# Kernel tuning notes

Measured on AMD Instinct MI355X. Metric: run time of the kernel, lower is better.

The kernel has to match this reference:

```python
import jax, jax.numpy as jnp
import numpy as np
import math

E = 1024   # embedding_size
H = 16     # layer_size (num heads)
DK = 64    # key_size
DH = 64    # head_size
HID = 4096 # hidden_size
B = 2
S = 2048   # context_size
EPS = 1e-5


def layer_norm(x, w, b):
    mu = jnp.mean(x, axis=-1, keepdims=True)
    var = jnp.mean(jnp.square(x - mu), axis=-1, keepdims=True)
    return (x - mu) * jax.lax.rsqrt(var + EPS) * w + b


def setup_inputs() -> dict:
    key = jax.random.key(0)
    ks = jax.random.split(key, 16)
    sE = 1.0 / math.sqrt(E)
    sH = 1.0 / math.sqrt(HID)
    return {
        "embeddings": jax.random.normal(ks[0], (B, S, E), dtype=jnp.float32),
        "Wq": jax.random.uniform(ks[1], (H, E, DK), minval=-sE, maxval=sE, dtype=jnp.float32),
        "bq": jnp.zeros((H, DK), dtype=jnp.float32),
        "Wk": jax.random.uniform(ks[2], (H, E, DK), minval=-sE, maxval=sE, dtype=jnp.float32),
        "bk": jnp.zeros((H, DK), dtype=jnp.float32),
        "Wv": jax.random.uniform(ks[3], (H, E, DH), minval=-sE, maxval=sE, dtype=jnp.float32),
        "bv": jnp.zeros((H, DH), dtype=jnp.float32),
        "ln1_w": jnp.ones((E,), dtype=jnp.float32),
        "ln1_b": jnp.zeros((E,), dtype=jnp.float32),
        "ln2_w": jnp.ones((E,), dtype=jnp.float32),
        "ln2_b": jnp.zeros((E,), dtype=jnp.float32),
        "W1": jax.random.uniform(ks[4], (E, HID), minval=-sE, maxval=sE, dtype=jnp.float32),
        "b1": jnp.zeros((HID,), dtype=jnp.float32),
        "W2": jax.random.uniform(ks[5], (HID, E), minval=-sH, maxval=sH, dtype=jnp.float32),
        "b2": jnp.zeros((E,), dtype=jnp.float32),
    }


def reference(embeddings, Wq, bq, Wk, bk, Wv, bv, ln1_w, ln1_b, ln2_w, ln2_b, W1, b1, W2, b2):
    # NOTE: faithful to source: residual uses the POST-norm activations
    # (embeddings is reassigned to the LayerNorm output before the residual add).
    x = layer_norm(embeddings, ln1_w, ln1_b)            # [B,S,E]
    q = jnp.einsum('bse,hed->bhsd', x, Wq) + bq[:, None, :]
    k = jnp.einsum('bse,hed->bhsd', x, Wk) + bk[:, None, :]
    v = jnp.einsum('bse,hed->bhsd', x, Wv) + bv[:, None, :]
    scores = jnp.einsum('bhsd,bhtd->bhst', q, k) / math.sqrt(DK)  # [B,H,S,S]
    causal = jnp.tril(jnp.ones((S, S), dtype=bool))
    scores = jnp.where(causal, scores, -jnp.inf)
    w = jax.nn.softmax(scores, axis=-1)
    o = jnp.einsum('bhst,bhtd->bhsd', w, v)             # [B,H,S,DH]
    o = jnp.transpose(o, (0, 2, 1, 3)).reshape(B, S, H * DH)  # concat heads
    x = x + o
    y = layer_norm(x, ln2_w, ln2_b)
    h = jax.nn.relu(jnp.einsum('bse,eh->bsh', y, W1) + b1)
    out = y + jnp.einsum('bsh,he->bse', h, W2) + b2
    return out
```

## Files before the change

### kernel.cpp

```cpp
#include <hip/hip_runtime.h>


typedef unsigned short u16;
typedef unsigned int   u32;
typedef __bf16 bf16x8 __attribute__((ext_vector_type(8)));
typedef float  f32x4  __attribute__((ext_vector_type(4)));

#define NEG_INF (-__builtin_inff())

__device__ __forceinline__ u16 f2b(float f) {
  u32 u = __float_as_uint(f);
  u = (u + 0x7fffu + ((u >> 16) & 1u)) >> 16;
  return (u16)u;
}

__device__ __forceinline__ void gload16(const void* g, void* l) {
  __builtin_amdgcn_global_load_lds(
      (const __attribute__((address_space(1))) u32*)g,
      (__attribute__((address_space(3))) u32*)l, 16, 0, 0);
}

__device__ __forceinline__ bf16x8 ld16(const u16* p) { return *(const bf16x8*)p; }

__global__ __launch_bounds__(256)
void transpose_bf16_k(const float* __restrict__ in, u16* __restrict__ out,
                      int R, int C) {
  __shared__ float tile[64][65];
  int r0 = blockIdx.x * 64, c0 = blockIdx.y * 64;
  const float* ip = in + (size_t)blockIdx.z * R * C;
  u16* op = out + (size_t)blockIdx.z * C * R;
  int tr = threadIdx.x >> 6, tc = threadIdx.x & 63;
#pragma unroll
  for (int i = 0; i < 16; i++) {
    int r = i * 4 + tr;
    tile[r][tc] = ip[(size_t)(r0 + r) * C + c0 + tc];
  }
  __syncthreads();
#pragma unroll
  for (int i = 0; i < 16; i++) {
    int c = i * 4 + tr;
    op[(size_t)(c0 + c) * R + r0 + tc] = f2b(tile[tc][c]);
  }
}

__global__ __launch_bounds__(256)
void vtrans_k(const u16* __restrict__ vin, u16* __restrict__ vt) {
  __shared__ __align__(16) u16 tile[64][72];
  int s0 = blockIdx.x * 64, bh = blockIdx.y;
  const u16* ip = vin + (size_t)bh * 2048 * 64;
  u16* op = vt + (size_t)bh * 64 * 2048;
  int t = threadIdx.x;
#pragma unroll
  for (int i = 0; i < 2; i++) {
    int idx = i * 256 + t, r = idx >> 3, c = idx & 7;
    *(uint4*)&tile[r][c * 8] = *(const uint4*)(ip + (size_t)(s0 + r) * 64 + c * 8);
  }
  __syncthreads();
#pragma unroll
  for (int i = 0; i < 16; i++) {
    int d = i * 4 + (t >> 6), s = t & 63;
    op[(size_t)d * 2048 + s0 + s] = tile[s][d];
  }
}

__global__ __launch_bounds__(256)
void ln_k(const float* __restrict__ in, const float* __restrict__ in2,
          const float* __restrict__ w, const float* __restrict__ b,
          float* __restrict__ outf, u16* __restrict__ outb) {
  int row = blockIdx.x, t = threadIdx.x;
  const float4* ip = (const float4*)(in + (size_t)row * 1024);
  float4 x = ip[t];
  if (in2) {
    const float4* ip2 = (const float4*)(in2 + (size_t)row * 1024);
    float4 o = ip2[t];
    x.x += o.x; x.y += o.y; x.z += o.z; x.w += o.w;
  }
  float s = x.x + x.y + x.z + x.w;
  float q = x.x * x.x + x.y * x.y + x.z * x.z + x.w * x.w;
#pragma unroll
  for (int m = 32; m; m >>= 1) { s += __shfl_xor(s, m); q += __shfl_xor(q, m); }
  __shared__ float rs[4], rq[4];
  if ((t & 63) == 0) { rs[t >> 6] = s; rq[t >> 6] = q; }
  __syncthreads();
  s = rs[0] + rs[1] + rs[2] + rs[3];
  q = rq[0] + rq[1] + rq[2] + rq[3];
  float mean = s * (1.f / 1024.f);
  float var  = q * (1.f / 1024.f) - mean * mean;
  float rstd = rsqrtf(var + 1e-5f);
  float4 wv = ((const float4*)w)[t];
  float4 bv = ((const float4*)b)[t];
  float4 y;
  y.x = (x.x - mean) * rstd * wv.x + bv.x;
  y.y = (x.y - mean) * rstd * wv.y + bv.y;
  y.z = (x.z - mean) * rstd * wv.z + bv.z;
  y.w = (x.w - mean) * rstd * wv.w + bv.w;
  if (outf) ((float4*)(outf + (size_t)row * 1024))[t] = y;
  ushort4 ub;
  ub.x = f2b(y.x); ub.y = f2b(y.y); ub.z = f2b(y.z); ub.w = f2b(y.w);
  ((ushort4*)(outb + (size_t)row * 1024))[t] = ub;
}

#define EPI_QKV  0
#define EPI_RELU 1
#define EPI_RES  2

#define QSCALE 0.18033688011112042f

template <int EPI>
__global__ __launch_bounds__(256)
void gemm_k(const u16* __restrict__ A, const u16* __restrict__ Bt,
            int K, int lda, int ldbt,
            const float* __restrict__ bias0, const float* __restrict__ bias1,
            const float* __restrict__ bias2, const float* __restrict__ res,
            int ldout, u16* __restrict__ outb, float* __restrict__ outf,
            float* __restrict__ outp) {
  __shared__ __align__(16) u16 As[128 * 64];
  __shared__ __align__(16) u16 Bs[128 * 64];
  int t = threadIdx.x;
  int wave = t >> 6, lane = t & 63, quad = lane >> 4, l16 = lane & 15;
  int x7 = l16 & 7;
  int wm = (wave >> 1) * 64, wn = (wave & 1) * 64;
  int bm = blockIdx.x * 128, bn = blockIdx.y * 128;
  int zoff = blockIdx.z * K;

  const u16* Agl[4];
  const u16* Bgl[4];
#pragma unroll
  for (int i = 0; i < 4; i++) {
    int idx = i * 256 + t, r = idx >> 3, c = (idx & 7) ^ (r & 7);
    Agl[i] = A + (size_t)(bm + r) * lda + zoff + c * 8;
    Bgl[i] = Bt + (size_t)(bn + r) * ldbt + zoff + c * 8;
  }
  u16* Asl = As + t * 8;
  u16* Bsl = Bs + t * 8;

  f32x4 acc[4][4] = {};

  for (int k0 = 0; k0 < K; k0 += 64) {
#pragma unroll
    for (int i = 0; i < 4; i++) {
      gload16(Agl[i] + k0, Asl + i * 2048);
      gload16(Bgl[i] + k0, Bsl + i * 2048);
    }
    __syncthreads();
#pragma unroll
    for (int kc = 0; kc < 2; kc++) {
      bf16x8 af[4], bfr[4];
#pragma unroll
      for (int i = 0; i < 4; i++) {
        int r = wm + i * 16 + l16;
        af[i] = *(const bf16x8*)(As + r * 64 + (((kc * 4 + quad) ^ x7) * 8));
      }
#pragma unroll
      for (int j = 0; j < 4; j++) {
        int r = wn + j * 16 + l16;
        bfr[j] = *(const bf16x8*)(Bs + r * 64 + (((kc * 4 + quad) ^ x7) * 8));
      }
#pragma unroll
      for (int i = 0; i < 4; i++)
#pragma unroll
        for (int j = 0; j < 4; j++)
          acc[i][j] = __builtin_amdgcn_mfma_f32_16x16x32_bf16(af[i], bfr[j],
                                                              acc[i][j], 0, 0, 0);
    }
    __syncthreads();
  }

#pragma unroll
  for (int i = 0; i < 4; i++) {
#pragma unroll
    for (int j = 0; j < 4; j++) {
      int c = bn + wn + j * 16 + l16;
#pragma unroll
      for (int rr = 0; rr < 4; rr++) {
        int r = bm + wm + i * 16 + quad * 4 + rr;
        float v = acc[i][j][rr];
        if (EPI == EPI_QKV) {
          int which = c >> 10, h = (c >> 6) & 15, d = c & 63;
          const float* bp = which == 0 ? bias0 : (which == 1 ? bias1 : bias2);
          v += bp[h * 64 + d];
          if (which == 0) v *= QSCALE;
          int bb = r >> 11, ss = r & 2047;
          outb[((size_t)(which * 32 + bb * 16 + h) * 2048 + ss) * 64 + d] = f2b(v);
        } else if (EPI == EPI_RELU) {
          v += bias0[c];
          v = v > 0.f ? v : 0.f;
          outb[(size_t)r * ldout + c] = f2b(v);
        } else {
          if (blockIdx.z == 0) {
            v += bias0[c] + res[(size_t)r * ldout + c];
            outf[(size_t)r * ldout + c] = v;
          } else {
            outp[(size_t)r * ldout + c] = v;
          }
        }
      }
    }
  }
}

__global__ __launch_bounds__(256)
void reduce_k(float* __restrict__ out, const float* __restrict__ part) {
  int i = blockIdx.x * 256 + threadIdx.x;
  float4 a = ((const float4*)part)[i];
  float4 b = ((float4*)out)[i];
  b.x += a.x; b.y += a.y; b.z += a.z; b.w += a.w;
  ((float4*)out)[i] = b;
}

__global__ __launch_bounds__(512, 6)
void attn_k(const u16* __restrict__ qkv, const u16* __restrict__ vt,
            float* __restrict__ o) {
  int bh = blockIdx.y, b = bh >> 4, h = bh & 15;
  int Qt = b ? (15 - (int)blockIdx.x) : (int)blockIdx.x;
  int t = threadIdx.x;
  int wave = t >> 6, lane = t & 63, quad = lane >> 4, l16 = lane & 15;
  int x7 = l16 & 7;
  int q0 = Qt * 128 + wave * 16;

  const u16* qg = qkv + (size_t)bh * (2048 * 64);
  const u16* kg = qkv + (size_t)(32 + bh) * (2048 * 64);
  const u16* vg = vt + (size_t)bh * (64 * 2048);

  __shared__ __align__(16) u16 Ks[2][64 * 64];
  __shared__ __align__(16) u16 Vs[2][64 * 64];
  __shared__ __align__(16) u16 Ps[8][16 * 64];
  u16* Pw = Ps[wave];

  int sr = t >> 3, sc_ = (t & 7) ^ (sr & 7);

  gload16(kg + (size_t)sr * 64 + sc_ * 8, Ks[0] + t * 8);
  gload16(vg + (size_t)sr * 2048 + sc_ * 8, Vs[0] + t * 8);

  bf16x8 qf0 = ld16(qg + (size_t)(q0 + l16) * 64 + quad * 8);
  bf16x8 qf1 = ld16(qg + (size_t)(q0 + l16) * 64 + 32 + quad * 8);

  f32x4 oacc[4] = {};
  float mo = NEG_INF, ll = 0.f;
  int kmax_w = q0 >> 6;
  int klast = 2 * Qt + 1;

  __syncthreads();

  for (int kt = 0; kt <= klast; kt++) {
    const u16* ks = Ks[kt & 1];
    const u16* vs = Vs[kt & 1];
    if (kt < klast) {
      gload16(kg + (size_t)((kt + 1) * 64 + sr) * 64 + sc_ * 8, Ks[(kt + 1) & 1] + t * 8);
      gload16(vg + (size_t)sr * 2048 + (kt + 1) * 64 + sc_ * 8, Vs[(kt + 1) & 1] + t * 8);
    }
    if (kt <= kmax_w) {
      f32x4 sc[4];
#pragma unroll
      for (int g = 0; g < 4; g++) {
        const u16* kr = ks + (g * 16 + l16) * 64;
        bf16x8 kf0 = *(const bf16x8*)(kr + ((quad ^ x7) * 8));
        bf16x8 kf1 = *(const bf16x8*)(kr + (((4 + quad) ^ x7) * 8));
        f32x4 s = {};
        s = __builtin_amdgcn_mfma_f32_16x16x32_bf16(kf0, qf0, s, 0, 0, 0);
        s = __builtin_amdgcn_mfma_f32_16x16x32_bf16(kf1, qf1, s, 0, 0, 0);
        sc[g] = s;
      }

      if (kt == kmax_w) {
#pragma unroll
        for (int g = 0; g < 4; g++) {
          int kvb = kt * 64 + g * 16 + quad * 4;
#pragma unroll
          for (int rr = 0; rr < 4; rr++)
            if (kvb + rr > q0 + l16) sc[g][rr] = NEG_INF;
        }
      }

      float mx = sc[0][0];
#pragma unroll
      for (int g = 0; g < 4; g++)
#pragma unroll
        for (int rr = 0; rr < 4; rr++) mx = fmaxf(mx, sc[g][rr]);
      mx = fmaxf(mx, __shfl_xor(mx, 16));
      mx = fmaxf(mx, __shfl_xor(mx, 32));
      float mnew = fmaxf(mo, mx);
      float al = exp2f(mo - mnew);
      mo = mnew;

      float sum = 0.f;
#pragma unroll
      for (int g = 0; g < 4; g++) {
        float p0 = exp2f(sc[g][0] - mnew);
        float p1 = exp2f(sc[g][1] - mnew);
        float p2 = exp2f(sc[g][2] - mnew);
        float p3 = exp2f(sc[g][3] - mnew);
        sum += (p0 + p1) + (p2 + p3);
        u32 lo = (__float_as_uint(p0) >> 16) | (__float_as_uint(p1) & 0xFFFF0000u);
        u32 hi = (__float_as_uint(p2) >> 16) | (__float_as_uint(p3) & 0xFFFF0000u);
        int slot = (2 * g + (quad >> 1)) ^ x7;
        *(uint2*)(Pw + l16 * 64 + slot * 8 + (quad & 1) * 4) = make_uint2(lo, hi);
      }
      sum += __shfl_xor(sum, 16);
      sum += __shfl_xor(sum, 32);
      ll = ll * al + sum;

#pragma unroll
      for (int rr = 0; rr < 4; rr++) {
        float ar = __shfl(al, quad * 20 + rr);
#pragma unroll
        for (int g = 0; g < 4; g++) oacc[g][rr] *= ar;
      }

      bf16x8 pf0 = *(const bf16x8*)(Pw + l16 * 64 + ((quad ^ x7) * 8));
      bf16x8 pf1 = *(const bf16x8*)(Pw + l16 * 64 + (((4 + quad) ^ x7) * 8));
#pragma unroll
      for (int g = 0; g < 4; g++) {
        const u16* vr = vs + (g * 16 + l16) * 64;
        bf16x8 vf0 = *(const bf16x8*)(vr + ((quad ^ x7) * 8));
        bf16x8 vf1 = *(const bf16x8*)(vr + (((4 + quad) ^ x7) * 8));
        oacc[g] = __builtin_amdgcn_mfma_f32_16x16x32_bf16(pf0, vf0, oacc[g], 0, 0, 0);
        oacc[g] = __builtin_amdgcn_mfma_f32_16x16x32_bf16(pf1, vf1, oacc[g], 0, 0, 0);
      }
    }
    __syncthreads();
  }

  float rinv[4];
#pragma unroll
  for (int rr = 0; rr < 4; rr++) rinv[rr] = 1.f / __shfl(ll, quad * 20 + rr);
  float* op = o + ((size_t)b * 2048 + q0) * 1024 + h * 64;
#pragma unroll
  for (int g = 0; g < 4; g++)
#pragma unroll
    for (int rr = 0; rr < 4; rr++)
      op[(size_t)(quad * 4 + rr) * 1024 + g * 16 + l16] = oacc[g][rr] * rinv[rr];
}

extern "C" void kernel_launch(void* const* d_in, const int* in_sizes, int n_in,
                              void* d_out, int out_size, void* d_ws, size_t ws_size,
                              hipStream_t stream) {
  const float* emb  = (const float*)d_in[0];
  const float* Wq   = (const float*)d_in[1];
  const float* bq   = (const float*)d_in[2];
  const float* Wk   = (const float*)d_in[3];
  const float* bk   = (const float*)d_in[4];
  const float* Wv   = (const float*)d_in[5];
  const float* bv   = (const float*)d_in[6];
  const float* ln1w = (const float*)d_in[7];
  const float* ln1b = (const float*)d_in[8];
  const float* ln2w = (const float*)d_in[9];
  const float* ln2b = (const float*)d_in[10];
  const float* W1   = (const float*)d_in[11];
  const float* b1   = (const float*)d_in[12];
  const float* W2   = (const float*)d_in[13];
  const float* b2   = (const float*)d_in[14];
  float* out = (float*)d_out;

  char* p = (char*)d_ws;
  u16*   Wqkv_t = (u16*)p;   p += (size_t)3072 * 1024 * 2;
  u16*   W1t    = (u16*)p;   p += (size_t)4096 * 1024 * 2;
  u16*   W2t    = (u16*)p;   p += (size_t)1024 * 4096 * 2;
  float* x      = (float*)p; p += (size_t)4096 * 1024 * 4;
  u16*   xb     = (u16*)p;   p += (size_t)4096 * 1024 * 2;
  u16*   qkvb   = (u16*)p;   p += (size_t)3 * 32 * 2048 * 64 * 2;
  float* ob     = (float*)p; p += (size_t)4096 * 1024 * 4;
  float* y      = (float*)p; p += (size_t)4096 * 1024 * 4;
  u16*   yb     = (u16*)p;   p += (size_t)4096 * 1024 * 2;
  u16*   hb     = (u16*)qkvb;
  u16*   vT     = (u16*)y;
  float* part   = x;
  if (ws_size < (size_t)(p - (char*)d_ws)) return;

  transpose_bf16_k<<<dim3(16, 1, 16), 256, 0, stream>>>(Wq, Wqkv_t,                   1024, 64);
  transpose_bf16_k<<<dim3(16, 1, 16), 256, 0, stream>>>(Wk, Wqkv_t + 1024 * 1024,     1024, 64);
  transpose_bf16_k<<<dim3(16, 1, 16), 256, 0, stream>>>(Wv, Wqkv_t + 2 * 1024 * 1024, 1024, 64);
  transpose_bf16_k<<<dim3(16, 64, 1), 256, 0, stream>>>(W1, W1t, 1024, 4096);
  transpose_bf16_k<<<dim3(64, 16, 1), 256, 0, stream>>>(W2, W2t, 4096, 1024);

  ln_k<<<dim3(4096), 256, 0, stream>>>(emb, nullptr, ln1w, ln1b, x, xb);

  gemm_k<EPI_QKV><<<dim3(32, 24, 1), 256, 0, stream>>>(
      xb, Wqkv_t, 1024, 1024, 1024, bq, bk, bv, nullptr, 0, qkvb, nullptr, nullptr);

  vtrans_k<<<dim3(32, 32), 256, 0, stream>>>(qkvb + (size_t)64 * 2048 * 64, vT);

  attn_k<<<dim3(16, 32), 512, 0, stream>>>(qkvb, vT, ob);

  ln_k<<<dim3(4096), 256, 0, stream>>>(x, ob, ln2w, ln2b, y, yb);

  gemm_k<EPI_RELU><<<dim3(32, 32, 1), 256, 0, stream>>>(
      yb, W1t, 1024, 1024, 1024, b1, nullptr, nullptr, nullptr, 4096, hb, nullptr, nullptr);

  gemm_k<EPI_RES><<<dim3(32, 8, 2), 256, 0, stream>>>(
      hb, W2t, 2048, 4096, 4096, b2, nullptr, nullptr, y, 1024, nullptr, out, part);

  reduce_k<<<dim3(4096), 256, 0, stream>>>(out, part);
}
```

Before: 357.4 us.

## Merge weight-transpose launches and cut softmax overhead in attention kernel

Merges the five weight transpose launches into two kernels, one for QKV and one for W1/W2, to reduce launch count. In attention, it uses the raw hardware exp2 builtin instead of exp2f, packs bf16 pairs with a perm instruction, and broadcasts row rescale factors through a small LDS area instead of cross-lane shuffles. The GEMM template is wrapped in separate kernels with narrower argument lists. The raw exp2 builtin skips range handling, which could slightly change precision for denormal inputs.

```diff
diff --git a/kernel.cpp b/kernel.cpp
--- a/kernel.cpp
+++ b/kernel.cpp
@@ -8,6 +8,20 @@
 
 #define NEG_INF (-__builtin_inff())
 
+#if __has_builtin(__builtin_amdgcn_exp2f)
+#define EXP2F(x) __builtin_amdgcn_exp2f(x)
+#else
+#define EXP2F(x) exp2f(x)
+#endif
+
+__device__ __forceinline__ u32 pack_bf16_trunc(float a, float b) {
+#if __has_builtin(__builtin_amdgcn_perm)
+  return __builtin_amdgcn_perm(__float_as_uint(b), __float_as_uint(a), 0x07060302u);
+#else
+  return (__float_as_uint(a) >> 16) | (__float_as_uint(b) & 0xFFFF0000u);
+#endif
+}
+
 __device__ __forceinline__ u16 f2b(float f) {
   u32 u = __float_as_uint(f);
   u = (u + 0x7fffu + ((u >> 16) & 1u)) >> 16;
@@ -23,23 +37,47 @@
 __device__ __forceinline__ bf16x8 ld16(const u16* p) { return *(const bf16x8*)p; }
 
 __global__ __launch_bounds__(256)
-void transpose_bf16_k(const float* __restrict__ in, u16* __restrict__ out,
-                      int R, int C) {
+void transpose_qkv_k(const float* __restrict__ Wq, const float* __restrict__ Wk,
+                     const float* __restrict__ Wv, u16* __restrict__ out) {
   __shared__ float tile[64][65];
-  int r0 = blockIdx.x * 64, c0 = blockIdx.y * 64;
-  const float* ip = in + (size_t)blockIdx.z * R * C;
-  u16* op = out + (size_t)blockIdx.z * C * R;
+  int z = blockIdx.z, which = z >> 4, sub = z & 15;
+  const float* in = which == 0 ? Wq : (which == 1 ? Wk : Wv);
+  const float* ip = in + (size_t)sub * 1024 * 64;
+  u16* op = out + (size_t)which * 1024 * 1024 + (size_t)sub * 64 * 1024;
+  int r0 = blockIdx.x * 64;
   int tr = threadIdx.x >> 6, tc = threadIdx.x & 63;
 #pragma unroll
   for (int i = 0; i < 16; i++) {
     int r = i * 4 + tr;
-    tile[r][tc] = ip[(size_t)(r0 + r) * C + c0 + tc];
+    tile[r][tc] = ip[(size_t)(r0 + r) * 64 + tc];
   }
   __syncthreads();
 #pragma unroll
   for (int i = 0; i < 16; i++) {
     int c = i * 4 + tr;
-    op[(size_t)(c0 + c) * R + r0 + tc] = f2b(tile[tc][c]);
+    op[(size_t)c * 1024 + r0 + tc] = f2b(tile[tc][c]);
+  }
+}
+
+__global__ __launch_bounds__(256)
+void transpose_w12_k(const float* __restrict__ W1, const float* __restrict__ W2,
+                     u16* __restrict__ W1t, u16* __restrict__ W2t) {
+  __shared__ float tile[64][65];
+  int id = blockIdx.x;
+  const float* in; u16* out; int R, C, r0, c0;
+  if (id < 1024) { in = W1; out = W1t; R = 1024; C = 4096; r0 = (id & 15) * 64; c0 = (id >> 4) * 64; }
+  else { id -= 1024; in = W2; out = W2t; R = 4096; C = 1024; r0 = (id >> 4) * 64; c0 = (id & 15) * 64; }
+  int tr = threadIdx.x >> 6, tc = threadIdx.x & 63;
+#pragma unroll
+  for (int i = 0; i < 16; i++) {
+    int r = i * 4 + tr;
+    tile[r][tc] = in[(size_t)(r0 + r) * C + c0 + tc];
+  }
+  __syncthreads();
+#pragma unroll
+  for (int i = 0; i < 16; i++) {
+    int c = i * 4 + tr;
+    out[(size_t)(c0 + c) * R + r0 + tc] = f2b(tile[tc][c]);
   }
 }
 
@@ -107,13 +145,13 @@
 #define QSCALE 0.18033688011112042f
 
 template <int EPI>
-__global__ __launch_bounds__(256)
-void gemm_k(const u16* __restrict__ A, const u16* __restrict__ Bt,
-            int K, int lda, int ldbt,
-            const float* __restrict__ bias0, const float* __restrict__ bias1,
-            const float* __restrict__ bias2, const float* __restrict__ res,
-            int ldout, u16* __restrict__ outb, float* __restrict__ outf,
-            float* __restrict__ outp) {
+__device__ __forceinline__
+void gemm_body(const u16* __restrict__ A, const u16* __restrict__ Bt,
+               int K, int lda, int ldbt,
+               const float* __restrict__ bias0, const float* __restrict__ bias1,
+               const float* __restrict__ bias2, const float* __restrict__ res,
+               int ldout, u16* __restrict__ outb, float* __restrict__ outf,
+               float* __restrict__ outp) {
   __shared__ __align__(16) u16 As[128 * 64];
   __shared__ __align__(16) u16 Bs[128 * 64];
   int t = threadIdx.x;
@@ -200,6 +238,24 @@
 }
 
 __global__ __launch_bounds__(256)
+void qkv_gemm(const u16* A, const u16* Bt, int K, int lda, int ldbt,
+              const float* b0, const float* b1, const float* b2,
+              u16* outb) {
+  gemm_body<EPI_QKV>(A, Bt, K, lda, ldbt, b0, b1, b2, nullptr, 0, outb, nullptr, nullptr);
+}
+__global__ __launch_bounds__(256)
+void ffn1_gemm(const u16* A, const u16* Bt, int K, int lda, int ldbt,
+               const float* b0, int ldout, u16* outb) {
+  gemm_body<EPI_RELU>(A, Bt, K, lda, ldbt, b0, nullptr, nullptr, nullptr, ldout, outb, nullptr, nullptr);
+}
+__global__ __launch_bounds__(256)
+void ffn2_gemm(const u16* A, const u16* Bt, int K, int lda, int ldbt,
+               const float* b0, const float* res, int ldout,
+               float* outf, float* outp) {
+  gemm_body<EPI_RES>(A, Bt, K, lda, ldbt, b0, nullptr, nullptr, res, ldout, nullptr, outf, outp);
+}
+
+__global__ __launch_bounds__(256)
 void reduce_k(float* __restrict__ out, const float* __restrict__ part) {
   int i = blockIdx.x * 256 + threadIdx.x;
   float4 a = ((const float4*)part)[i];
@@ -224,8 +280,9 @@
 
   __shared__ __align__(16) u16 Ks[2][64 * 64];
   __shared__ __align__(16) u16 Vs[2][64 * 64];
-  __shared__ __align__(16) u16 Ps[8][16 * 64];
+  __shared__ __align__(16) u16 Ps[8][16 * 64 + 32];
   u16* Pw = Ps[wave];
+  float* auxf = (float*)(Pw + 1024);
 
   int sr = t >> 3, sc_ = (t & 7) ^ (sr & 7);
 
@@ -280,19 +337,19 @@
       mx = fmaxf(mx, __shfl_xor(mx, 16));
       mx = fmaxf(mx, __shfl_xor(mx, 32));
       float mnew = fmaxf(mo, mx);
-      float al = exp2f(mo - mnew);
+      float al = EXP2F(mo - mnew);
       mo = mnew;
 
       float sum = 0.f;
 #pragma unroll
       for (int g = 0; g < 4; g++) {
-        float p0 = exp2f(sc[g][0] - mnew);
-        float p1 = exp2f(sc[g][1] - mnew);
-        float p2 = exp2f(sc[g][2] - mnew);
-        float p3 = exp2f(sc[g][3] - mnew);
+        float p0 = EXP2F(sc[g][0] - mnew);
+        float p1 = EXP2F(sc[g][1] - mnew);
+        float p2 = EXP2F(sc[g][2] - mnew);
+        float p3 = EXP2F(sc[g][3] - mnew);
         sum += (p0 + p1) + (p2 + p3);
-        u32 lo = (__float_as_uint(p0) >> 16) | (__float_as_uint(p1) & 0xFFFF0000u);
-        u32 hi = (__float_as_uint(p2) >> 16) | (__float_as_uint(p3) & 0xFFFF0000u);
+        u32 lo = pack_bf16_trunc(p0, p1);
+        u32 hi = pack_bf16_trunc(p2, p3);
         int slot = (2 * g + (quad >> 1)) ^ x7;
         *(uint2*)(Pw + l16 * 64 + slot * 8 + (quad & 1) * 4) = make_uint2(lo, hi);
       }
@@ -300,12 +357,12 @@
       sum += __shfl_xor(sum, 32);
       ll = ll * al + sum;
 
-#pragma unroll
-      for (int rr = 0; rr < 4; rr++) {
-        float ar = __shfl(al, quad * 20 + rr);
-#pragma unroll
-        for (int g = 0; g < 4; g++) oacc[g][rr] *= ar;
-      }
+      if (lane < 16) auxf[lane] = al;
+      f32x4 av = *(const f32x4*)(auxf + quad * 4);
+#pragma unroll
+      for (int g = 0; g < 4; g++)
+#pragma unroll
+        for (int rr = 0; rr < 4; rr++) oacc[g][rr] *= av[rr];
 
       bf16x8 pf0 = *(const bf16x8*)(Pw + l16 * 64 + ((quad ^ x7) * 8));
       bf16x8 pf1 = *(const bf16x8*)(Pw + l16 * 64 + (((4 + quad) ^ x7) * 8));
@@ -321,9 +378,11 @@
     __syncthreads();
   }
 
+  if (lane < 16) auxf[lane] = ll;
+  f32x4 lv = *(const f32x4*)(auxf + quad * 4);
   float rinv[4];
 #pragma unroll
-  for (int rr = 0; rr < 4; rr++) rinv[rr] = 1.f / __shfl(ll, quad * 20 + rr);
+  for (int rr = 0; rr < 4; rr++) rinv[rr] = 1.f / lv[rr];
   float* op = o + ((size_t)b * 2048 + q0) * 1024 + h * 64;
 #pragma unroll
   for (int g = 0; g < 4; g++)
@@ -367,16 +426,13 @@
   float* part   = x;
   if (ws_size < (size_t)(p - (char*)d_ws)) return;
 
-  transpose_bf16_k<<<dim3(16, 1, 16), 256, 0, stream>>>(Wq, Wqkv_t,                   1024, 64);
-  transpose_bf16_k<<<dim3(16, 1, 16), 256, 0, stream>>>(Wk, Wqkv_t + 1024 * 1024,     1024, 64);
-  transpose_bf16_k<<<dim3(16, 1, 16), 256, 0, stream>>>(Wv, Wqkv_t + 2 * 1024 * 1024, 1024, 64);
-  transpose_bf16_k<<<dim3(16, 64, 1), 256, 0, stream>>>(W1, W1t, 1024, 4096);
-  transpose_bf16_k<<<dim3(64, 16, 1), 256, 0, stream>>>(W2, W2t, 4096, 1024);
+  transpose_qkv_k<<<dim3(16, 1, 48), 256, 0, stream>>>(Wq, Wk, Wv, Wqkv_t);
+  transpose_w12_k<<<dim3(2048), 256, 0, stream>>>(W1, W2, W1t, W2t);
 
   ln_k<<<dim3(4096), 256, 0, stream>>>(emb, nullptr, ln1w, ln1b, x, xb);
 
-  gemm_k<EPI_QKV><<<dim3(32, 24, 1), 256, 0, stream>>>(
-      xb, Wqkv_t, 1024, 1024, 1024, bq, bk, bv, nullptr, 0, qkvb, nullptr, nullptr);
+  qkv_gemm<<<dim3(32, 24, 1), 256, 0, stream>>>(
+      xb, Wqkv_t, 1024, 1024, 1024, bq, bk, bv, qkvb);
 
   vtrans_k<<<dim3(32, 32), 256, 0, stream>>>(qkvb + (size_t)64 * 2048 * 64, vT);
 
@@ -384,11 +440,11 @@
 
   ln_k<<<dim3(4096), 256, 0, stream>>>(x, ob, ln2w, ln2b, y, yb);
 
-  gemm_k<EPI_RELU><<<dim3(32, 32, 1), 256, 0, stream>>>(
-      yb, W1t, 1024, 1024, 1024, b1, nullptr, nullptr, nullptr, 4096, hb, nullptr, nullptr);
-
-  gemm_k<EPI_RES><<<dim3(32, 8, 2), 256, 0, stream>>>(
-      hb, W2t, 2048, 4096, 4096, b2, nullptr, nullptr, y, 1024, nullptr, out, part);
+  ffn1_gemm<<<dim3(32, 32, 1), 256, 0, stream>>>(
+      yb, W1t, 1024, 1024, 1024, b1, 4096, hb);
+
+  ffn2_gemm<<<dim3(32, 8, 2), 256, 0, stream>>>(
+      hb, W2t, 2048, 4096, 4096, b2, y, 1024, out, part);
 
   reduce_k<<<dim3(4096), 256, 0, stream>>>(out, part);
 }
```

Measured after the change: 333.1 us. -6.8%, faster.
